# Kernel tuning notes

Measured on AMD Instinct MI355X. Metric: run time of the kernel, lower is better.

Reference implementation:

```python
import jax, jax.numpy as jnp
import numpy as np

V = 1.0e10           # large init value for non-seed pixels (FastGeodis v)
LAMB = 0.0           # lamb=0 => pure Euclidean raster-scan distance
ITERS = 2            # FastGeodis iterations
THRESH = 0.7         # binarize_map threshold
TOPO_WEIGHT = 0.005
TOPO_WINDOW = 64
EPS = 1e-6
BIG = 1e20


def _sweep_down(dist, image):
    # One top-down raster sweep of the FastGeodis up-down pass.
    # dist, image: [H, W]. Row r updates from row r-1 at col offsets {-1,0,+1}
    # with squared spatial distances {2,1,2}; lamb weights the intensity term.
    W = dist.shape[1]
    sp2 = (2.0, 1.0, 2.0)

    def step(carry, xs):
        pd, pi = carry          # previous-row distance / intensity, [W]
        d_row, i_row = xs
        pd_pad = jnp.pad(pd, 1, constant_values=BIG)
        pi_pad = jnp.pad(pi, 1, constant_values=0.0)
        new = d_row
        for k in range(3):
            p = pd_pad[k:k + W]
            q = i_row - pi_pad[k:k + W]
            new = jnp.minimum(new, p + jnp.sqrt(sp2[k] + LAMB * q * q))
        return (new, i_row), new

    (_, _), rest = jax.lax.scan(step, (dist[0], image[0]), (dist[1:], image[1:]))
    return jnp.concatenate([dist[:1], rest], axis=0)


def _updown(dist, image):
    dist = _sweep_down(dist, image)
    dist = _sweep_down(dist[::-1], image[::-1])[::-1]
    return dist


def generalised_geodesic2d(image, softmask):
    # image: intensity map [H,W]; softmask: [H,W]; dist init = V * softmask.
    dist = V * softmask
    for _ in range(ITERS):
        dist = _updown(dist, image)
        dist = _updown(dist.T, image.T).T
    return dist


def calculate_edt(inp):
    # Original: softmask = inp, intensity image = 1 - inp (mask_pt = 1 - image_pt).
    return generalised_geodesic2d(1.0 - inp, inp)


def _global_norm(x):
    return (x - x.min()) / (x.max() - x.min() + EPS)


def _topo_loss(p, t, window):
    # Persistence-style matching proxy: within each non-overlapping window,
    # match level-set values of pred and target by sorting (0-dim persistence
    # birth/death values of the filtration are order statistics of the window)
    # and penalize squared differences of matched values.
    H, W = p.shape
    nh, nw = H // window, W // window

    def win_sort(x):
        x = x.reshape(nh, window, nw, window).transpose(0, 2, 1, 3)
        return jnp.sort(x.reshape(nh * nw, window * window), axis=-1)

    return jnp.mean((win_sort(p) - win_sort(t)) ** 2)


def _per_item(pred_i, target_i):
    # pred_i/target_i: [C, H, W]; pred already remapped to [0, 1]
    bin_pred = (pred_i >= THRESH).astype(jnp.float32)
    comb_pred = jnp.max(bin_pred, axis=0)        # combine_channels
    comb_tgt = jnp.max(target_i, axis=0)
    edt_p = _global_norm(calculate_edt(1.0 - comb_pred))
    edt_t = _global_norm(calculate_edt(1.0 - comb_tgt))
    return _topo_loss(edt_p, edt_t, TOPO_WINDOW)


def setup_inputs():
    key = jax.random.key(0)
    k1, k2 = jax.random.split(key)
    B, C, H, W = 16, 3, 512, 512
    pred = jax.random.normal(k1, (B, C, H, W), dtype=jnp.float32)  # model output in ~[-1,1]
    # target: binary multi-channel cell masks (sparse foreground)
    target = (jax.random.uniform(k2, (B, C, H, W)) > 0.8).astype(jnp.float32)
    return {"pred": pred, "target": target}


def reference(pred, target):
    pred01 = (pred + 1.0) / 2.0
    losses = jax.vmap(_per_item)(pred01.astype(jnp.float32), target.astype(jnp.float32))
    mean_loss = losses.mean()
    return (mean_loss * TOPO_WEIGHT, mean_loss)
```

## Files before the change

### kernel.cpp

```cpp
#include <hip/hip_runtime.h>

#define BIGF 1e20f
#define VF   1e10f

constexpr float SQ2 = 1.41421356237309515f;

__device__ __forceinline__ float dpp_left(float x)
{
    int o = __builtin_amdgcn_update_dpp(0x60AD78ECu , __float_as_int(x),
                                        0x138, 0xF, 0xF, false);
    return __int_as_float(o);
}
__device__ __forceinline__ float dpp_right(float x)
{
    int o = __builtin_amdgcn_update_dpp(0x60AD78ECu , __float_as_int(x),
                                        0x130, 0xF, 0xF, false);
    return __int_as_float(o);
}
template<int CTRL>
__device__ __forceinline__ float qdpp(float x)
{
    return __int_as_float(__builtin_amdgcn_update_dpp(0, __float_as_int(x),
                                                      CTRL, 0xF, 0xF, true));
}
__device__ __forceinline__ float fmed3(float a, float b, float c)
{
    return __builtin_amdgcn_fmed3f(a, b, c);
}

__device__ __forceinline__ void load_row8(const float* __restrict__ M, int r, int c0, float v[8])
{
    const float4* q = (const float4*)(M + ((long)r << 9) + c0);
    float4 a = q[0], b = q[1];
    v[0] = a.x; v[1] = a.y; v[2] = a.z; v[3] = a.w;
    v[4] = b.x; v[5] = b.y; v[6] = b.z; v[7] = b.w;
}
__device__ __forceinline__ void store_row8(float* __restrict__ M, int r, int c0, const float v[8])
{
    float4* q = (float4*)(M + ((long)r << 9) + c0);
    q[0] = make_float4(v[0], v[1], v[2], v[3]);
    q[1] = make_float4(v[4], v[5], v[6], v[7]);
}

__device__ __forceinline__ void step8(const float cur[8], const float p[8], float nv[8])
{
    float left  = dpp_left(p[7]);
    float right = dpp_right(p[0]);
    #pragma unroll
    for (int j = 0; j < 8; ++j) {
        float l  = (j == 0) ? left  : p[j - 1];
        float rr = (j == 7) ? right : p[j + 1];
        nv[j] = fminf(fminf(cur[j], p[j] + 1.0f), fminf(l, rr) + SQ2);
    }
}

__global__ __launch_bounds__(256) void k_init(const float* __restrict__ pred,
                                              const float* __restrict__ tgt,
                                              float* __restrict__ bufA,
                                              float* __restrict__ acc,
                                              unsigned* __restrict__ count,
                                              float* __restrict__ minmax)
{
    if (blockIdx.x == 0 && threadIdx.x == 0) { *acc = 0.0f; *count = 0u; }
    if (blockIdx.x == 0 && threadIdx.x < 64)
        minmax[threadIdx.x] = (threadIdx.x & 1) ? 0.0f : BIGF;

    int r = blockIdx.x & 7;
    int k = blockIdx.x >> 3;
    int b = r + 8 * (k >> 10);
    int pix = (k & 1023) * 256 + threadIdx.x;
    long base = (long)b * 3 * 262144 + pix;

    float p0 = pred[base], p1 = pred[base + 262144], p2 = pred[base + 2 * 262144];
    bool fgP = ((p0 + 1.0f) * 0.5f >= 0.7f) ||
               ((p1 + 1.0f) * 0.5f >= 0.7f) ||
               ((p2 + 1.0f) * 0.5f >= 0.7f);

    float t0 = tgt[base], t1 = tgt[base + 262144], t2 = tgt[base + 2 * 262144];
    float mt = fmaxf(fmaxf(t0, t1), t2);

    bufA[(long)b * 262144 + pix]        = fgP ? 0.0f : VF;
    bufA[(long)(16 + b) * 262144 + pix] = VF * (1.0f - mt);
}

__global__ __launch_bounds__(64) void k_p1d(const float* __restrict__ X0,
                                            float* __restrict__ Cb)
{
    int bi = blockIdx.x, m = bi >> 4, w = bi & 15;
    const float* X = X0 + ((long)m << 18);
    int c0 = (int)threadIdx.x << 3, a = w << 5;
    float p[8]; load_row8(X, a, c0, p);
    float buf[8][8];
    #pragma unroll
    for (int k = 1; k <= 7; ++k) load_row8(X, a + k, c0, buf[k & 7]);
    #pragma unroll
    for (int i = 1; i < 32; ++i) {
        if (i + 7 < 32) load_row8(X, a + i + 7, c0, buf[(i + 7) & 7]);
        float nv[8]; step8(buf[i & 7], p, nv);
        #pragma unroll
        for (int j = 0; j < 8; ++j) p[j] = nv[j];
    }
    float4* o = (float4*)(Cb + m * 8192 + w * 512 + c0);
    o[0] = make_float4(p[0], p[1], p[2], p[3]);
    o[1] = make_float4(p[4], p[5], p[6], p[7]);
}

__device__ __forceinline__ void combine(float* __restrict__ bwp, float* __restrict__ part,
                                        int wdst, int wsrc, int t, int wave, int lane,
                                        const float wreg[8])
{
    const float* bs = bwp + wsrc * 576;
    if (wave <= 8) {
        int base = lane * 8 + 8 * wave;
        float W[16];
        float4 W0 = *(const float4*)(bs + base);
        float4 W1 = *(const float4*)(bs + base + 4);
        W[0]=W0.x; W[1]=W0.y; W[2]=W0.z; W[3]=W0.w;
        W[4]=W1.x; W[5]=W1.y; W[6]=W1.z; W[7]=W1.w;
        float acc[8];
        if (wave < 8) {
            float4 W2 = *(const float4*)(bs + base + 8);
            float4 W3 = *(const float4*)(bs + base + 12);
            W[8]=W2.x; W[9]=W2.y; W[10]=W2.z; W[11]=W2.w;
            W[12]=W3.x; W[13]=W3.y; W[14]=W3.z; W[15]=W3.w;
            #pragma unroll
            for (int j = 0; j < 8; ++j) acc[j] = W[j] + wreg[0];
            #pragma unroll
            for (int dt = 1; dt < 8; ++dt)
                #pragma unroll
                for (int j = 0; j < 8; ++j)
                    acc[j] = fminf(acc[j], W[j + dt] + wreg[dt]);
        } else {
            #pragma unroll
            for (int j = 0; j < 8; ++j) acc[j] = W[j] + wreg[0];
        }
        float4* pp = (float4*)(part + wave * 512 + lane * 8);
        pp[0] = make_float4(acc[0], acc[1], acc[2], acc[3]);
        pp[1] = make_float4(acc[4], acc[5], acc[6], acc[7]);
    }
    __syncthreads();
    if (t < 512) {
        float r = bwp[wdst * 576 + 32 + t];
        #pragma unroll
        for (int p2 = 0; p2 < 9; ++p2) r = fminf(r, part[p2 * 512 + t]);
        bwp[wdst * 576 + 32 + t] = r;
    }
    __syncthreads();
}

__global__ __launch_bounds__(1024) void k_comb(float* __restrict__ Cb, int dir)
{
    __shared__ __align__(16) float bwp[16 * 576];
    __shared__ __align__(16) float part[9 * 512];
    __shared__ float wgt[72];
    int m = blockIdx.x, t = threadIdx.x, wave = t >> 6, lane = t & 63, c0 = lane << 3;
    float* Cm = Cb + m * 8192;

    bwp[wave * 576 + ((lane < 32) ? lane : lane + 512)] = BIGF;
    *(float4*)(bwp + wave * 576 + 32 + c0)     = *(const float4*)(Cm + wave * 512 + c0);
    *(float4*)(bwp + wave * 576 + 32 + c0 + 4) = *(const float4*)(Cm + wave * 512 + c0 + 4);
    if (t < 65) { int d = t - 32; int ad = d < 0 ? -d : d; wgt[t] = ad * SQ2 + (float)(32 - ad); }
    __syncthreads();
    float wreg[8];
    #pragma unroll
    for (int dt = 0; dt < 8; ++dt) wreg[dt] = BIGF;
    if (wave < 8) {
        #pragma unroll
        for (int dt = 0; dt < 8; ++dt) wreg[dt] = wgt[wave * 8 + dt];
    } else if (wave == 8) wreg[0] = wgt[64];

    #pragma unroll 1
    for (int i = 0; i < 15; ++i) {
        int w2 = (dir > 0) ? (1 + i) : (14 - i);
        combine(bwp, part, w2, w2 - dir, t, wave, lane, wreg);
    }
    *(float4*)(Cm + wave * 512 + c0)     = *(const float4*)(bwp + wave * 576 + 32 + c0);
    *(float4*)(Cm + wave * 512 + c0 + 4) = *(const float4*)(bwp + wave * 576 + 32 + c0 + 4);
}

__global__ __launch_bounds__(64) void k_p3d1u(const float* __restrict__ X0,
                                              float* __restrict__ Y0,
                                              const float* __restrict__ Cb,
                                              float* __restrict__ Db)
{
    __shared__ __align__(16) float stash[31 * 512];
    int bi = blockIdx.x, m = bi >> 4, w = bi & 15;
    const float* X = X0 + ((long)m << 18);
    float* Y = Y0 + ((long)m << 18);
    const int L = threadIdx.x;
    int c0 = L << 3, a = w << 5;
    float p[8], buf[8][8];

    if (w == 0) {
        load_row8(X, 0, c0, p);
        store_row8(Y, 0, c0, p);
        *(float4*)(stash + 0 * 512 + L * 4)       = make_float4(p[0], p[1], p[2], p[3]);
        *(float4*)(stash + 0 * 512 + 256 + L * 4) = make_float4(p[4], p[5], p[6], p[7]);
        #pragma unroll
        for (int k = 1; k <= 7; ++k) load_row8(X, k, c0, buf[k & 7]);
        #pragma unroll
        for (int i = 1; i < 32; ++i) {
            if (i + 7 < 32) load_row8(X, i + 7, c0, buf[(i + 7) & 7]);
            float nv[8]; step8(buf[i & 7], p, nv);
            store_row8(Y, i, c0, nv);
            if (i < 31) {
                *(float4*)(stash + i * 512 + L * 4)       = make_float4(nv[0], nv[1], nv[2], nv[3]);
                *(float4*)(stash + i * 512 + 256 + L * 4) = make_float4(nv[4], nv[5], nv[6], nv[7]);
            }
            #pragma unroll
            for (int j = 0; j < 8; ++j) p[j] = nv[j];
        }
    } else {
        const float4* s = (const float4*)(Cb + m * 8192 + (w - 1) * 512 + c0);
        float4 s0 = s[0], s1 = s[1];
        p[0]=s0.x; p[1]=s0.y; p[2]=s0.z; p[3]=s0.w;
        p[4]=s1.x; p[5]=s1.y; p[6]=s1.z; p[7]=s1.w;
        #pragma unroll
        for (int k = 0; k < 7; ++k) load_row8(X, a + k, c0, buf[k & 7]);
        #pragma unroll
        for (int i = 0; i < 32; ++i) {
            if (i + 7 < 32) load_row8(X, a + i + 7, c0, buf[(i + 7) & 7]);
            float nv[8]; step8(buf[i & 7], p, nv);
            store_row8(Y, a + i, c0, nv);
            if (i < 31) {
                *(float4*)(stash + i * 512 + L * 4)       = make_float4(nv[0], nv[1], nv[2], nv[3]);
                *(float4*)(stash + i * 512 + 256 + L * 4) = make_float4(nv[4], nv[5], nv[6], nv[7]);
            }
            #pragma unroll
            for (int j = 0; j < 8; ++j) p[j] = nv[j];
        }
    }

    float q[8], cur[8];
    #pragma unroll
    for (int j = 0; j < 8; ++j) q[j] = p[j];
    {
        float4 x0 = *(const float4*)(stash + 30 * 512 + L * 4);
        float4 x1 = *(const float4*)(stash + 30 * 512 + 256 + L * 4);
        cur[0]=x0.x; cur[1]=x0.y; cur[2]=x0.z; cur[3]=x0.w;
        cur[4]=x1.x; cur[5]=x1.y; cur[6]=x1.z; cur[7]=x1.w;
    }
    #pragma unroll
    for (int i = 1; i < 32; ++i) {
        float nxt[8];
        if (i < 31) {
            float4 x0 = *(const float4*)(stash + (30 - i) * 512 + L * 4);
            float4 x1 = *(const float4*)(stash + (30 - i) * 512 + 256 + L * 4);
            nxt[0]=x0.x; nxt[1]=x0.y; nxt[2]=x0.z; nxt[3]=x0.w;
            nxt[4]=x1.x; nxt[5]=x1.y; nxt[6]=x1.z; nxt[7]=x1.w;
        }
        float nv[8]; step8(cur, q, nv);
        #pragma unroll
        for (int j = 0; j < 8; ++j) q[j] = nv[j];
        if (i < 31) {
            #pragma unroll
            for (int j = 0; j < 8; ++j) cur[j] = nxt[j];
        }
    }
    float4* o = (float4*)(Db + m * 8192 + w * 512 + c0);
    o[0] = make_float4(q[0], q[1], q[2], q[3]);
    o[1] = make_float4(q[4], q[5], q[6], q[7]);
}

__device__ __forceinline__ void tile_store(float* tile, int h, int c0, const float v[8])
{
    float4* q = (float4*)(tile + h * 516 + c0);
    q[0] = make_float4(v[0], v[1], v[2], v[3]);
    q[1] = make_float4(v[4], v[5], v[6], v[7]);
}
__device__ __forceinline__ void half_out(const float* tile, float* __restrict__ Xo,
                                         int a2, int L)
{
    int g = L >> 2, j = (L & 3) << 2;
    #pragma unroll
    for (int it = 0; it < 32; ++it) {
        int c = (it << 4) + g;
        float4 v = make_float4(tile[(j + 0) * 516 + c], tile[(j + 1) * 516 + c],
                               tile[(j + 2) * 516 + c], tile[(j + 3) * 516 + c]);
        *(float4*)(Xo + (long)c * 512 + a2 + j) = v;
    }
}

__global__ __launch_bounds__(64) void k_p3u(const float* __restrict__ Y0,
                                            float* __restrict__ Xo0,
                                            const float* __restrict__ Db,
                                            float* __restrict__ minmax,
                                            int final_pass)
{
    __shared__ __align__(16) float tile[16 * 516];
    int bi = blockIdx.x, m = bi >> 4, w = bi & 15;
    const float* Y = Y0 + ((long)m << 18);
    float* Xo = Xo0 + ((long)m << 18);
    int L = threadIdx.x, c0 = L << 3, a = w << 5;
    float p[8], buf[8][8];
    float mn = BIGF, mx = -BIGF;

    if (w == 15) {
        load_row8(Y, 511, c0, p);
        tile_store(tile, 15, c0, p);
        #pragma unroll
        for (int j = 0; j < 8; ++j) { mn = fminf(mn, p[j]); mx = fmaxf(mx, p[j]); }
        #pragma unroll
        for (int k = 1; k <= 7; ++k) load_row8(Y, 511 - k, c0, buf[k & 7]);
        #pragma unroll
        for (int i = 1; i < 16; ++i) {
            if (i + 7 < 32) load_row8(Y, 511 - (i + 7), c0, buf[(i + 7) & 7]);
            float nv[8]; step8(buf[i & 7], p, nv);
            tile_store(tile, 15 - i, c0, nv);
            #pragma unroll
            for (int j = 0; j < 8; ++j) { p[j] = nv[j]; mn = fminf(mn, nv[j]); mx = fmaxf(mx, nv[j]); }
        }
        half_out(tile, Xo, a + 16, L);
        #pragma unroll
        for (int i = 16; i < 32; ++i) {
            if (i + 7 < 32) load_row8(Y, 511 - (i + 7), c0, buf[(i + 7) & 7]);
            float nv[8]; step8(buf[i & 7], p, nv);
            tile_store(tile, 31 - i, c0, nv);
            #pragma unroll
            for (int j = 0; j < 8; ++j) { p[j] = nv[j]; mn = fminf(mn, nv[j]); mx = fmaxf(mx, nv[j]); }
        }
        half_out(tile, Xo, a, L);
    } else {
        const float4* s = (const float4*)(Db + m * 8192 + (w + 1) * 512 + c0);
        float4 s0 = s[0], s1 = s[1];
        p[0]=s0.x; p[1]=s0.y; p[2]=s0.z; p[3]=s0.w;
        p[4]=s1.x; p[5]=s1.y; p[6]=s1.z; p[7]=s1.w;
        #pragma unroll
        for (int k = 0; k < 7; ++k) load_row8(Y, a + 31 - k, c0, buf[k & 7]);
        #pragma unroll
        for (int i = 0; i < 16; ++i) {
            if (i + 7 < 32) load_row8(Y, a + 31 - (i + 7), c0, buf[(i + 7) & 7]);
            float nv[8]; step8(buf[i & 7], p, nv);
            tile_store(tile, 15 - i, c0, nv);
            #pragma unroll
            for (int j = 0; j < 8; ++j) { p[j] = nv[j]; mn = fminf(mn, nv[j]); mx = fmaxf(mx, nv[j]); }
        }
        half_out(tile, Xo, a + 16, L);
        #pragma unroll
        for (int i = 16; i < 32; ++i) {
            if (i + 7 < 32) load_row8(Y, a + 31 - (i + 7), c0, buf[(i + 7) & 7]);
            float nv[8]; step8(buf[i & 7], p, nv);
            tile_store(tile, 31 - i, c0, nv);
            #pragma unroll
            for (int j = 0; j < 8; ++j) { p[j] = nv[j]; mn = fminf(mn, nv[j]); mx = fmaxf(mx, nv[j]); }
        }
        half_out(tile, Xo, a, L);
    }

    if (final_pass) {
        for (int o = 32; o > 0; o >>= 1) {
            mn = fminf(mn, __shfl_down(mn, o));
            mx = fmaxf(mx, __shfl_down(mx, o));
        }
        if (L == 0) {
            atomicMin((int*)(minmax + 2 * m),     __float_as_int(mn));
            atomicMax((int*)(minmax + 2 * m + 1), __float_as_int(mx));
        }
    }
}

__device__ __forceinline__ void cex(float& lo, float& hi)
{
    float l = fminf(lo, hi);
    hi = fmaxf(lo, hi);
    lo = l;
}
__device__ __forceinline__ void merge8asc(float v[8])
{
    cex(v[0],v[4]); cex(v[1],v[5]); cex(v[2],v[6]); cex(v[3],v[7]);
    cex(v[0],v[2]); cex(v[1],v[3]); cex(v[4],v[6]); cex(v[5],v[7]);
    cex(v[0],v[1]); cex(v[2],v[3]); cex(v[4],v[5]); cex(v[6],v[7]);
}
__device__ __forceinline__ void sort8asc(float v[8])
{
    cex(v[0],v[1]); cex(v[2],v[3]); cex(v[4],v[5]); cex(v[6],v[7]);
    cex(v[0],v[3]); cex(v[1],v[2]); cex(v[4],v[7]); cex(v[5],v[6]);
    cex(v[0],v[1]); cex(v[2],v[3]); cex(v[4],v[5]); cex(v[6],v[7]);
    cex(v[0],v[7]); cex(v[1],v[6]); cex(v[2],v[5]); cex(v[3],v[4]);
    cex(v[0],v[2]); cex(v[1],v[3]); cex(v[4],v[6]); cex(v[5],v[7]);
    cex(v[0],v[1]); cex(v[2],v[3]); cex(v[4],v[5]); cex(v[6],v[7]);
}
__device__ __forceinline__ void xshfl(float v[8], int j8, float sel)
{
    #pragma unroll
    for (int e = 0; e < 8; ++e) {
        float o = __shfl_xor(v[e], j8);
        v[e] = fmed3(v[e], o, sel);
// ... 127 lines not shown
    float s = 0.0f;
    #pragma unroll
    for (int e = 0; e < 8; ++e) { float d = p[e] - q[e]; s += d * d; }
    for (int o = 32; o > 0; o >>= 1) s += __shfl_down(s, o);
    if ((t & 63) == 0) rs[t >> 6] = s;
    __syncthreads();
    if (t == 0) {
        float tot = 0.0f;
        #pragma unroll
        for (int i = 0; i < 8; ++i) tot += rs[i];
        atomicAdd(acc, tot);
        __threadfence();
        unsigned done = atomicAdd(count, 1u);
        if (done == 1023u) {
            float total = atomicAdd(acc, 0.0f);
            float mean = total * (1.0f / 4194304.0f);
            out[0] = mean * 0.005f;
            out[1] = mean;
        }
    }
}

extern "C" void kernel_launch(void* const* d_in, const int* in_sizes, int n_in,
                              void* d_out, int out_size, void* d_ws, size_t ws_size,
                              hipStream_t stream)
{
    const float* pred = (const float*)d_in[0];
    const float* tgt  = (const float*)d_in[1];
    float* out = (float*)d_out;

    char* ws = (char*)d_ws;
    float* bufA     = (float*)ws;
    float* bufB     = (float*)(ws + (32ull << 20));
    float* Cb       = (float*)(ws + (64ull << 20));
    float* Db       = (float*)(ws + (65ull << 20));
    float* minmax   = (float*)(ws + (66ull << 20));
    float* acc      = minmax + 64;
    unsigned* count = (unsigned*)(acc + 1);

    k_init<<<16 * 1024, 256, 0, stream>>>(pred, tgt, bufA, acc, count, minmax);

    for (int s = 0; s < 4; ++s) {
        k_p1d  <<<512,   64, 0, stream>>>(bufA, Cb);
        k_comb <<< 32, 1024, 0, stream>>>(Cb, +1);
        k_p3d1u<<<512,   64, 0, stream>>>(bufA, bufB, Cb, Db);
        k_comb <<< 32, 1024, 0, stream>>>(Db, -1);
        k_p3u  <<<512,   64, 0, stream>>>(bufB, bufA, Db, minmax, s == 3 ? 1 : 0);
    }

    k_loss<<<1024, 512, 0, stream>>>(bufA, minmax, acc, count, out);
}
```

Measured before the change: 406.6 us.

## Fuse per-pass sweep kernels into one persistent kernel with inter-block flag sync

Replaces the five kernels per pass (block-local sweep, two block-boundary combine kernels, down and up sweeps) with a single kernel. Blocks publish boundary rows through atomics and spin on global flags, and block 0 of each image runs the cross-block cone combine serially. Intermediate rows are kept in LDS instead of being written to and re-read from a global buffer. This removes launch overhead and global round trips, but depends on all 512 blocks being co-resident to avoid deadlock, and adds serial spin latency plus atomic traffic.

```diff
diff --git a/kernel.cpp b/kernel.cpp
--- a/kernel.cpp
+++ b/kernel.cpp
@@ -35,12 +35,6 @@
     v[0] = a.x; v[1] = a.y; v[2] = a.z; v[3] = a.w;
     v[4] = b.x; v[5] = b.y; v[6] = b.z; v[7] = b.w;
 }
-__device__ __forceinline__ void store_row8(float* __restrict__ M, int r, int c0, const float v[8])
-{
-    float4* q = (float4*)(M + ((long)r << 9) + c0);
-    q[0] = make_float4(v[0], v[1], v[2], v[3]);
-    q[1] = make_float4(v[4], v[5], v[6], v[7]);
-}
 
 __device__ __forceinline__ void step8(const float cur[8], const float p[8], float nv[8])
 {
@@ -51,6 +45,100 @@
         float l  = (j == 0) ? left  : p[j - 1];
         float rr = (j == 7) ? right : p[j + 1];
         nv[j] = fminf(fminf(cur[j], p[j] + 1.0f), fminf(l, rr) + SQ2);
+    }
+}
+
+__device__ __forceinline__ void sst_(float* st, int slot, int c0, const float v[8])
+{
+    float4* q = (float4*)(st + slot * 512 + c0);
+    q[0] = make_float4(v[0], v[1], v[2], v[3]);
+    q[1] = make_float4(v[4], v[5], v[6], v[7]);
+}
+__device__ __forceinline__ void sld_(const float* st, int slot, int c0, float v[8])
+{
+    const float4* q = (const float4*)(st + slot * 512 + c0);
+    float4 a = q[0], b = q[1];
+    v[0]=a.x; v[1]=a.y; v[2]=a.z; v[3]=a.w;
+    v[4]=b.x; v[5]=b.y; v[6]=b.z; v[7]=b.w;
+}
+
+__device__ __forceinline__ void pub_row(float* dst, int c0, const float v[8])
+{
+    #pragma unroll
+    for (int j = 0; j < 8; ++j) atomicExch(&dst[c0 + j], v[j]);
+}
+__device__ __forceinline__ void rd_row(float* src, int c0, float v[8])
+{
+    #pragma unroll
+    for (int j = 0; j < 8; ++j) v[j] = atomicAdd(&src[c0 + j], 0.0f);
+}
+
+__device__ __forceinline__ void spin_ge(unsigned* f, unsigned tgt)
+{
+    unsigned v = 0;
+    int iters = 0;
+    do {
+        if (threadIdx.x == 0) v = atomicAdd(f, 0u);
+        v = (unsigned)__shfl((int)v, 0);
+        if (v >= tgt) break;
+        __builtin_amdgcn_s_sleep(8);
+    } while (++iters < (1 << 21));
+}
+
+__device__ constexpr float coneWf(int t)
+{
+    int ad = (t < 32) ? (32 - t) : (t - 32);
+    return (float)ad * 1.41421356237309515f + (float)(32 - ad);
+}
+
+__device__ __forceinline__ void cone32_step(float prev[8], const float bw[8],
+                                            float* scratch, int L)
+{
+    int c0 = L << 3;
+    *(float4*)(scratch + c0)     = make_float4(prev[0], prev[1], prev[2], prev[3]);
+    *(float4*)(scratch + c0 + 4) = make_float4(prev[4], prev[5], prev[6], prev[7]);
+    float o[8];
+    #pragma unroll
+    for (int j = 0; j < 8; ++j) o[j] = bw[j];
+    #pragma unroll
+    for (int k = 0; k < 9; ++k) {
+        int blk = L - 4 + k;
+        bool ok = (blk >= 0) && (blk < 64);
+        int off = (ok ? blk : 0) << 3;
+        float4 x0 = *(const float4*)(scratch + off);
+        float4 x1 = *(const float4*)(scratch + off + 4);
+        float wv[8] = {x0.x, x0.y, x0.z, x0.w, x1.x, x1.y, x1.z, x1.w};
+        #pragma unroll
+        for (int e = 0; e < 8; ++e) {
+            float val = ok ? wv[e] : BIGF;
+            #pragma unroll
+            for (int j = 0; j < 8; ++j) {
+                const int t = (k - 4) * 8 + e - j + 32;
+                if (t >= 0 && t <= 64)
+                    o[j] = fminf(o[j], val + coneWf(t));
+            }
+        }
+    }
+    #pragma unroll
+    for (int j = 0; j < 8; ++j) prev[j] = o[j];
+}
+
+template<int PERM>
+__device__ __forceinline__ void half_out2(const float* st, float* __restrict__ Xo,
+                                          int a2, int L)
+{
+    int g = L >> 2, j = (L & 3) << 2;
+    #pragma unroll
+    for (int it = 0; it < 32; ++it) {
+        int c = (it << 4) + g;
+        float v[4];
+        #pragma unroll
+        for (int kk = 0; kk < 4; ++kk) {
+            int h = j + kk;
+            int slot = PERM ? ((h + 15) & 15) : (15 + h);
+            v[kk] = st[slot * 512 + c];
+        }
+        *(float4*)(Xo + (long)c * 512 + a2 + j) = make_float4(v[0], v[1], v[2], v[3]);
     }
 }
 
@@ -59,11 +147,15 @@
                                               float* __restrict__ bufA,
                                               float* __restrict__ acc,
                                               unsigned* __restrict__ count,
-                                              float* __restrict__ minmax)
+                                              float* __restrict__ minmax,
+                                              unsigned* __restrict__ flags)
 {
     if (blockIdx.x == 0 && threadIdx.x == 0) { *acc = 0.0f; *count = 0u; }
     if (blockIdx.x == 0 && threadIdx.x < 64)
         minmax[threadIdx.x] = (threadIdx.x & 1) ? 0.0f : BIGF;
+    if (blockIdx.x == 0) {
+        for (int i = threadIdx.x; i < 2048; i += 256) flags[i] = 0u;
+    }
 
     int r = blockIdx.x & 7;
     int k = blockIdx.x >> 3;
@@ -83,269 +175,157 @@
     bufA[(long)(16 + b) * 262144 + pix] = VF * (1.0f - mt);
 }
 
-__global__ __launch_bounds__(64) void k_p1d(const float* __restrict__ X0,
-                                            float* __restrict__ Cb)
-{
+__global__ __launch_bounds__(64) void k_pass(const float* __restrict__ Xin0,
+                                             float* __restrict__ Xout0,
+                                             float* __restrict__ bnd,
+                                             float* __restrict__ scn,
+                                             unsigned* __restrict__ flags,
+                                             float* __restrict__ minmax,
+                                             int pi, int final_pass)
+{
+    __shared__ __align__(16) float stash[31 * 512 + 512];
+    float* scratch = stash + 31 * 512;
+
     int bi = blockIdx.x, m = bi >> 4, w = bi & 15;
-    const float* X = X0 + ((long)m << 18);
-    int c0 = (int)threadIdx.x << 3, a = w << 5;
-    float p[8]; load_row8(X, a, c0, p);
-    float buf[8][8];
-    #pragma unroll
-    for (int k = 1; k <= 7; ++k) load_row8(X, a + k, c0, buf[k & 7]);
-    #pragma unroll
-    for (int i = 1; i < 32; ++i) {
-        if (i + 7 < 32) load_row8(X, a + i + 7, c0, buf[(i + 7) & 7]);
-        float nv[8]; step8(buf[i & 7], p, nv);
-        #pragma unroll
-        for (int j = 0; j < 8; ++j) p[j] = nv[j];
-    }
-    float4* o = (float4*)(Cb + m * 8192 + w * 512 + c0);
-    o[0] = make_float4(p[0], p[1], p[2], p[3]);
-    o[1] = make_float4(p[4], p[5], p[6], p[7]);
-}
-
-__device__ __forceinline__ void combine(float* __restrict__ bwp, float* __restrict__ part,
-                                        int wdst, int wsrc, int t, int wave, int lane,
-                                        const float wreg[8])
-{
-    const float* bs = bwp + wsrc * 576;
-    if (wave <= 8) {
-        int base = lane * 8 + 8 * wave;
-        float W[16];
-        float4 W0 = *(const float4*)(bs + base);
-        float4 W1 = *(const float4*)(bs + base + 4);
-        W[0]=W0.x; W[1]=W0.y; W[2]=W0.z; W[3]=W0.w;
-        W[4]=W1.x; W[5]=W1.y; W[6]=W1.z; W[7]=W1.w;
-        float acc[8];
-        if (wave < 8) {
-            float4 W2 = *(const float4*)(bs + base + 8);
-            float4 W3 = *(const float4*)(bs + base + 12);
-            W[8]=W2.x; W[9]=W2.y; W[10]=W2.z; W[11]=W2.w;
-            W[12]=W3.x; W[13]=W3.y; W[14]=W3.z; W[15]=W3.w;
-            #pragma unroll
-            for (int j = 0; j < 8; ++j) acc[j] = W[j] + wreg[0];
-            #pragma unroll
-            for (int dt = 1; dt < 8; ++dt)
-                #pragma unroll
-                for (int j = 0; j < 8; ++j)
-                    acc[j] = fminf(acc[j], W[j + dt] + wreg[dt]);
-        } else {
-            #pragma unroll
-            for (int j = 0; j < 8; ++j) acc[j] = W[j] + wreg[0];
-        }
-        float4* pp = (float4*)(part + wave * 512 + lane * 8);
-        pp[0] = make_float4(acc[0], acc[1], acc[2], acc[3]);
-        pp[1] = make_float4(acc[4], acc[5], acc[6], acc[7]);
-    }
-    __syncthreads();
-    if (t < 512) {
-        float r = bwp[wdst * 576 + 32 + t];
-        #pragma unroll
-        for (int p2 = 0; p2 < 9; ++p2) r = fminf(r, part[p2 * 512 + t]);
-        bwp[wdst * 576 + 32 + t] = r;
-    }
-    __syncthreads();
-}
-
-__global__ __launch_bounds__(1024) void k_comb(float* __restrict__ Cb, int dir)
-{
-    __shared__ __align__(16) float bwp[16 * 576];
-    __shared__ __align__(16) float part[9 * 512];
-    __shared__ float wgt[72];
-    int m = blockIdx.x, t = threadIdx.x, wave = t >> 6, lane = t & 63, c0 = lane << 3;
-    float* Cm = Cb + m * 8192;
-
-    bwp[wave * 576 + ((lane < 32) ? lane : lane + 512)] = BIGF;
-    *(float4*)(bwp + wave * 576 + 32 + c0)     = *(const float4*)(Cm + wave * 512 + c0);
-    *(float4*)(bwp + wave * 576 + 32 + c0 + 4) = *(const float4*)(Cm + wave * 512 + c0 + 4);
-    if (t < 65) { int d = t - 32; int ad = d < 0 ? -d : d; wgt[t] = ad * SQ2 + (float)(32 - ad); }
-    __syncthreads();
-    float wreg[8];
-    #pragma unroll
-    for (int dt = 0; dt < 8; ++dt) wreg[dt] = BIGF;
-    if (wave < 8) {
-        #pragma unroll
-        for (int dt = 0; dt < 8; ++dt) wreg[dt] = wgt[wave * 8 + dt];
-    } else if (wave == 8) wreg[0] = wgt[64];
-
-    #pragma unroll 1
-    for (int i = 0; i < 15; ++i) {
-        int w2 = (dir > 0) ? (1 + i) : (14 - i);
-        combine(bwp, part, w2, w2 - dir, t, wave, lane, wreg);
-    }
-    *(float4*)(Cm + wave * 512 + c0)     = *(const float4*)(bwp + wave * 576 + 32 + c0);
-    *(float4*)(Cm + wave * 512 + c0 + 4) = *(const float4*)(bwp + wave * 576 + 32 + c0 + 4);
-}
-
-__global__ __launch_bounds__(64) void k_p3d1u(const float* __restrict__ X0,
-                                              float* __restrict__ Y0,
-                                              const float* __restrict__ Cb,
-                                              float* __restrict__ Db)
-{
-    __shared__ __align__(16) float stash[31 * 512];
-    int bi = blockIdx.x, m = bi >> 4, w = bi & 15;
-    const float* X = X0 + ((long)m << 18);
-    float* Y = Y0 + ((long)m << 18);
+    const float* X = Xin0 + ((long)m << 18);
+    float* Xo = Xout0 + ((long)m << 18);
     const int L = threadIdx.x;
     int c0 = L << 3, a = w << 5;
-    float p[8], buf[8][8];
+    unsigned* fl = flags + (((pi << 5) | m) << 4);
+    float* bndm = bnd + (m << 13);
+    float* scnm = scn + (m << 13);
+
+    float p[8], row0[8], buf[8][8];
+
+    load_row8(X, a, c0, p);
+    #pragma unroll
+    for (int j = 0; j < 8; ++j) row0[j] = p[j];
+    #pragma unroll
+    for (int k = 1; k <= 7; ++k) {
+        load_row8(X, a + k, c0, buf[k & 7]);
+        if (w) sst_(stash, k - 1, c0, buf[k & 7]);
+    }
+    #pragma unroll
+    for (int i = 1; i < 32; ++i) {
+        if (i + 7 < 32) {
+            load_row8(X, a + i + 7, c0, buf[(i + 7) & 7]);
+            if (w) sst_(stash, i + 6, c0, buf[(i + 7) & 7]);
+        }
+        float nv[8]; step8(buf[i & 7], p, nv);
+        if (!w) sst_(stash, i - 1, c0, nv);
+        #pragma unroll
+        for (int j = 0; j < 8; ++j) p[j] = nv[j];
+    }
+    pub_row(bndm + (w << 9), c0, p);
+    __threadfence();
+    if (L == 0) atomicAdd(&fl[0], 1u);
 
     if (w == 0) {
-        load_row8(X, 0, c0, p);
-        store_row8(Y, 0, c0, p);
-        *(float4*)(stash + 0 * 512 + L * 4)       = make_float4(p[0], p[1], p[2], p[3]);
-        *(float4*)(stash + 0 * 512 + 256 + L * 4) = make_float4(p[4], p[5], p[6], p[7]);
-        #pragma unroll
-        for (int k = 1; k <= 7; ++k) load_row8(X, k, c0, buf[k & 7]);
-        #pragma unroll
+        spin_ge(&fl[0], 16u);
+        __threadfence();
+        float prev[8];
+        #pragma unroll
+        for (int j = 0; j < 8; ++j) prev[j] = p[j];
+        pub_row(scnm, c0, prev);
+        __threadfence();
+        if (L == 0) atomicExch(&fl[1], 1u);
+        #pragma unroll 1
+        for (int wp = 1; wp <= 14; ++wp) {
+            float bw[8]; rd_row(bndm + (wp << 9), c0, bw);
+            cone32_step(prev, bw, scratch, L);
+            pub_row(scnm + (wp << 9), c0, prev);
+            __threadfence();
+            if (L == 0) atomicExch(&fl[1], (unsigned)(wp + 1));
+        }
+    } else {
+        spin_ge(&fl[1], (unsigned)w);
+        __threadfence();
+        rd_row(scnm + ((w - 1) << 9), c0, p);
+        {
+            float nv[8]; step8(row0, p, nv);
+            #pragma unroll
+            for (int j = 0; j < 8; ++j) { row0[j] = nv[j]; p[j] = nv[j]; }
+        }
+        #pragma unroll 1
         for (int i = 1; i < 32; ++i) {
-            if (i + 7 < 32) load_row8(X, i + 7, c0, buf[(i + 7) & 7]);
-            float nv[8]; step8(buf[i & 7], p, nv);
-            store_row8(Y, i, c0, nv);
-            if (i < 31) {
-                *(float4*)(stash + i * 512 + L * 4)       = make_float4(nv[0], nv[1], nv[2], nv[3]);
-                *(float4*)(stash + i * 512 + 256 + L * 4) = make_float4(nv[4], nv[5], nv[6], nv[7]);
-            }
+            float cu[8]; sld_(stash, i - 1, c0, cu);
+            float nv[8]; step8(cu, p, nv);
+            sst_(stash, i - 1, c0, nv);
             #pragma unroll
             for (int j = 0; j < 8; ++j) p[j] = nv[j];
         }
+    }
+
+    float q[8];
+    #pragma unroll
+    for (int j = 0; j < 8; ++j) q[j] = p[j];
+    #pragma unroll 1
+    for (int i = 1; i < 32; ++i) {
+        float cu[8];
+        if (i < 31) sld_(stash, 30 - i, c0, cu);
+        else {
+            #pragma unroll
+            for (int j = 0; j < 8; ++j) cu[j] = row0[j];
+        }
+        float nv[8]; step8(cu, q, nv);
+        #pragma unroll
+        for (int j = 0; j < 8; ++j) q[j] = nv[j];
+    }
+    spin_ge(&fl[1], 15u);
+    pub_row(bndm + (w << 9), c0, q);
+    __threadfence();
+    if (L == 0) atomicAdd(&fl[2], 1u);
+
+    if (w == 0) {
+        spin_ge(&fl[2], 16u);
+        __threadfence();
+        float prev[8]; rd_row(bndm + (15 << 9), c0, prev);
+        pub_row(scnm + (15 << 9), c0, prev);
+        __threadfence();
+        if (L == 0) atomicExch(&fl[3], 1u);
+        #pragma unroll 1
+        for (int wp = 14; wp >= 1; --wp) {
+            float bw[8]; rd_row(bndm + (wp << 9), c0, bw);
+            cone32_step(prev, bw, scratch, L);
+            pub_row(scnm + (wp << 9), c0, prev);
+            __threadfence();
+            if (L == 0) atomicExch(&fl[3], (unsigned)(16 - wp));
+        }
+    }
+
+    float s2[8];
+    if (w == 15) {
+        #pragma unroll
+        for (int j = 0; j < 8; ++j) s2[j] = BIGF;
     } else {
-        const float4* s = (const float4*)(Cb + m * 8192 + (w - 1) * 512 + c0);
-        float4 s0 = s[0], s1 = s[1];
-        p[0]=s0.x; p[1]=s0.y; p[2]=s0.z; p[3]=s0.w;
-        p[4]=s1.x; p[5]=s1.y; p[6]=s1.z; p[7]=s1.w;
-        #pragma unroll
-        for (int k = 0; k < 7; ++k) load_row8(X, a + k, c0, buf[k & 7]);
-        #pragma unroll
-        for (int i = 0; i < 32; ++i) {
-            if (i + 7 < 32) load_row8(X, a + i + 7, c0, buf[(i + 7) & 7]);
-            float nv[8]; step8(buf[i & 7], p, nv);
-            store_row8(Y, a + i, c0, nv);
-            if (i < 31) {
-                *(float4*)(stash + i * 512 + L * 4)       = make_float4(nv[0], nv[1], nv[2], nv[3]);
-                *(float4*)(stash + i * 512 + 256 + L * 4) = make_float4(nv[4], nv[5], nv[6], nv[7]);
-            }
+        spin_ge(&fl[3], (unsigned)(15 - w));
+        __threadfence();
+        rd_row(scnm + ((w + 1) << 9), c0, s2);
+    }
+    float mn = BIGF, mx = -BIGF;
+    #pragma unroll 1
+    for (int i = 0; i < 16; ++i) {
+        float cu[8]; sld_(stash, 30 - i, c0, cu);
+        float nv[8]; step8(cu, s2, nv);
+        sst_(stash, 30 - i, c0, nv);
+        #pragma unroll
+        for (int j = 0; j < 8; ++j) { s2[j] = nv[j]; mn = fminf(mn, nv[j]); mx = fmaxf(mx, nv[j]); }
+    }
+    half_out2<0>(stash, Xo, a + 16, L);
+    #pragma unroll 1
+    for (int i = 16; i < 32; ++i) {
+        float cu[8];
+        if (i < 31) sld_(stash, 30 - i, c0, cu);
+        else {
             #pragma unroll
-            for (int j = 0; j < 8; ++j) p[j] = nv[j];
-        }
-    }
-
-    float q[8], cur[8];
-    #pragma unroll
-    for (int j = 0; j < 8; ++j) q[j] = p[j];
-    {
-        float4 x0 = *(const float4*)(stash + 30 * 512 + L * 4);
-        float4 x1 = *(const float4*)(stash + 30 * 512 + 256 + L * 4);
-        cur[0]=x0.x; cur[1]=x0.y; cur[2]=x0.z; cur[3]=x0.w;
-        cur[4]=x1.x; cur[5]=x1.y; cur[6]=x1.z; cur[7]=x1.w;
-    }
-    #pragma unroll
-    for (int i = 1; i < 32; ++i) {
-        float nxt[8];
-        if (i < 31) {
-            float4 x0 = *(const float4*)(stash + (30 - i) * 512 + L * 4);
-            float4 x1 = *(const float4*)(stash + (30 - i) * 512 + 256 + L * 4);
-            nxt[0]=x0.x; nxt[1]=x0.y; nxt[2]=x0.z; nxt[3]=x0.w;
-            nxt[4]=x1.x; nxt[5]=x1.y; nxt[6]=x1.z; nxt[7]=x1.w;
-        }
-        float nv[8]; step8(cur, q, nv);
-        #pragma unroll
-        for (int j = 0; j < 8; ++j) q[j] = nv[j];
-        if (i < 31) {
-            #pragma unroll
-            for (int j = 0; j < 8; ++j) cur[j] = nxt[j];
-        }
-    }
-    float4* o = (float4*)(Db + m * 8192 + w * 512 + c0);
-    o[0] = make_float4(q[0], q[1], q[2], q[3]);
-    o[1] = make_float4(q[4], q[5], q[6], q[7]);
-}
-
-__device__ __forceinline__ void tile_store(float* tile, int h, int c0, const float v[8])
-{
-    float4* q = (float4*)(tile + h * 516 + c0);
-    q[0] = make_float4(v[0], v[1], v[2], v[3]);
-    q[1] = make_float4(v[4], v[5], v[6], v[7]);
-}
-__device__ __forceinline__ void half_out(const float* tile, float* __restrict__ Xo,
-                                         int a2, int L)
-{
-    int g = L >> 2, j = (L & 3) << 2;
-    #pragma unroll
-    for (int it = 0; it < 32; ++it) {
-        int c = (it << 4) + g;
-        float4 v = make_float4(tile[(j + 0) * 516 + c], tile[(j + 1) * 516 + c],
-                               tile[(j + 2) * 516 + c], tile[(j + 3) * 516 + c]);
-        *(float4*)(Xo + (long)c * 512 + a2 + j) = v;
-    }
-}
-
-__global__ __launch_bounds__(64) void k_p3u(const float* __restrict__ Y0,
-                                            float* __restrict__ Xo0,
-                                            const float* __restrict__ Db,
-                                            float* __restrict__ minmax,
-                                            int final_pass)
-{
-    __shared__ __align__(16) float tile[16 * 516];
-    int bi = blockIdx.x, m = bi >> 4, w = bi & 15;
-    const float* Y = Y0 + ((long)m << 18);
-    float* Xo = Xo0 + ((long)m << 18);
-    int L = threadIdx.x, c0 = L << 3, a = w << 5;
-    float p[8], buf[8][8];
-    float mn = BIGF, mx = -BIGF;
-
-    if (w == 15) {
-        load_row8(Y, 511, c0, p);
-        tile_store(tile, 15, c0, p);
-        #pragma unroll
-        for (int j = 0; j < 8; ++j) { mn = fminf(mn, p[j]); mx = fmaxf(mx, p[j]); }
-        #pragma unroll
-        for (int k = 1; k <= 7; ++k) load_row8(Y, 511 - k, c0, buf[k & 7]);
-        #pragma unroll
-        for (int i = 1; i < 16; ++i) {
-            if (i + 7 < 32) load_row8(Y, 511 - (i + 7), c0, buf[(i + 7) & 7]);
-            float nv[8]; step8(buf[i & 7], p, nv);
-            tile_store(tile, 15 - i, c0, nv);
-            #pragma unroll
-            for (int j = 0; j < 8; ++j) { p[j] = nv[j]; mn = fminf(mn, nv[j]); mx = fmaxf(mx, nv[j]); }
-        }
-        half_out(tile, Xo, a + 16, L);
-        #pragma unroll
-        for (int i = 16; i < 32; ++i) {
-            if (i + 7 < 32) load_row8(Y, 511 - (i + 7), c0, buf[(i + 7) & 7]);
-            float nv[8]; step8(buf[i & 7], p, nv);
-            tile_store(tile, 31 - i, c0, nv);
-            #pragma unroll
-            for (int j = 0; j < 8; ++j) { p[j] = nv[j]; mn = fminf(mn, nv[j]); mx = fmaxf(mx, nv[j]); }
-        }
-        half_out(tile, Xo, a, L);
-    } else {
-        const float4* s = (const float4*)(Db + m * 8192 + (w + 1) * 512 + c0);
-        float4 s0 = s[0], s1 = s[1];
-        p[0]=s0.x; p[1]=s0.y; p[2]=s0.z; p[3]=s0.w;
-        p[4]=s1.x; p[5]=s1.y; p[6]=s1.z; p[7]=s1.w;
-        #pragma unroll
-        for (int k = 0; k < 7; ++k) load_row8(Y, a + 31 - k, c0, buf[k & 7]);
-        #pragma unroll
-        for (int i = 0; i < 16; ++i) {
-            if (i + 7 < 32) load_row8(Y, a + 31 - (i + 7), c0, buf[(i + 7) & 7]);
-            float nv[8]; step8(buf[i & 7], p, nv);
-            tile_store(tile, 15 - i, c0, nv);
-            #pragma unroll
-            for (int j = 0; j < 8; ++j) { p[j] = nv[j]; mn = fminf(mn, nv[j]); mx = fmaxf(mx, nv[j]); }
-        }
-        half_out(tile, Xo, a + 16, L);
-        #pragma unroll
-        for (int i = 16; i < 32; ++i) {
-            if (i + 7 < 32) load_row8(Y, a + 31 - (i + 7), c0, buf[(i + 7) & 7]);
-            float nv[8]; step8(buf[i & 7], p, nv);
-            tile_store(tile, 31 - i, c0, nv);
-            #pragma unroll
-            for (int j = 0; j < 8; ++j) { p[j] = nv[j]; mn = fminf(mn, nv[j]); mx = fmaxf(mx, nv[j]); }
-        }
-        half_out(tile, Xo, a, L);
-    }
+            for (int j = 0; j < 8; ++j) cu[j] = row0[j];
+        }
+        float nv[8]; step8(cu, s2, nv);
+        sst_(stash, (i < 31) ? (30 - i) : 15, c0, nv);
+        #pragma unroll
+        for (int j = 0; j < 8; ++j) { s2[j] = nv[j]; mn = fminf(mn, nv[j]); mx = fmaxf(mx, nv[j]); }
+    }
+    half_out2<1>(stash, Xo, a, L);
 
     if (final_pass) {
         for (int o = 32; o > 0; o >>= 1) {
@@ -546,20 +526,19 @@
     char* ws = (char*)d_ws;
     float* bufA     = (float*)ws;
     float* bufB     = (float*)(ws + (32ull << 20));
-    float* Cb       = (float*)(ws + (64ull << 20));
-    float* Db       = (float*)(ws + (65ull << 20));
+    float* bnd      = (float*)(ws + (64ull << 20));
+    float* scn      = (float*)(ws + (65ull << 20));
     float* minmax   = (float*)(ws + (66ull << 20));
     float* acc      = minmax + 64;
     unsigned* count = (unsigned*)(acc + 1);
-
-    k_init<<<16 * 1024, 256, 0, stream>>>(pred, tgt, bufA, acc, count, minmax);
+    unsigned* flags = (unsigned*)(ws + (66ull << 20) + 512);
+
+    k_init<<<16 * 1024, 256, 0, stream>>>(pred, tgt, bufA, acc, count, minmax, flags);
 
     for (int s = 0; s < 4; ++s) {
-        k_p1d  <<<512,   64, 0, stream>>>(bufA, Cb);
-        k_comb <<< 32, 1024, 0, stream>>>(Cb, +1);
-        k_p3d1u<<<512,   64, 0, stream>>>(bufA, bufB, Cb, Db);
-        k_comb <<< 32, 1024, 0, stream>>>(Db, -1);
-        k_p3u  <<<512,   64, 0, stream>>>(bufB, bufA, Db, minmax, s == 3 ? 1 : 0);
+        const float* in = (s & 1) ? bufB : bufA;
+        float* outb     = (s & 1) ? bufA : bufB;
+        k_pass<<<512, 64, 0, stream>>>(in, outb, bnd, scn, flags, minmax, s, (s == 3) ? 1 : 0);
     }
 
     k_loss<<<1024, 512, 0, stream>>>(bufA, minmax, acc, count, out);
```

Result: slower. 1.303 ms (+220.5%).

## Spread each row sweep across four waves with LDS halo exchange

Applied to the files above, without the earlier changes.

The three sweep kernels now use 256 threads per block, each handling 2 columns instead of one 64-lane wave handling 8 columns per lane. Neighbouring-column values at wave boundaries are exchanged through a small double-buffered shared-memory array, with a __syncthreads every row step. The aim is more parallelism and latency hiding per block with fewer serial ALU ops per lane, at the cost of a block-wide barrier on every one of the 32+ sequential row steps.

```diff
diff --git a/kernel.cpp b/kernel.cpp
--- a/kernel.cpp
+++ b/kernel.cpp
@@ -28,30 +28,29 @@
     return __builtin_amdgcn_fmed3f(a, b, c);
 }
 
-__device__ __forceinline__ void load_row8(const float* __restrict__ M, int r, int c0, float v[8])
-{
-    const float4* q = (const float4*)(M + ((long)r << 9) + c0);
-    float4 a = q[0], b = q[1];
-    v[0] = a.x; v[1] = a.y; v[2] = a.z; v[3] = a.w;
-    v[4] = b.x; v[5] = b.y; v[6] = b.z; v[7] = b.w;
-}
-__device__ __forceinline__ void store_row8(float* __restrict__ M, int r, int c0, const float v[8])
-{
-    float4* q = (float4*)(M + ((long)r << 9) + c0);
-    q[0] = make_float4(v[0], v[1], v[2], v[3]);
-    q[1] = make_float4(v[4], v[5], v[6], v[7]);
-}
-
-__device__ __forceinline__ void step8(const float cur[8], const float p[8], float nv[8])
-{
-    float left  = dpp_left(p[7]);
-    float right = dpp_right(p[0]);
-    #pragma unroll
-    for (int j = 0; j < 8; ++j) {
-        float l  = (j == 0) ? left  : p[j - 1];
-        float rr = (j == 7) ? right : p[j + 1];
-        nv[j] = fminf(fminf(cur[j], p[j] + 1.0f), fminf(l, rr) + SQ2);
-    }
+__device__ __forceinline__ void step2(const float cur[2], const float p[2],
+                                      float nv[2], float left, float right)
+{
+    nv[0] = fminf(fminf(cur[0], p[0] + 1.0f), fminf(left, p[1]) + SQ2);
+    nv[1] = fminf(fminf(cur[1], p[1] + 1.0f), fminf(p[0], right) + SQ2);
+}
+
+__device__ __forceinline__ void halo_exchange(float* hs, int pb, int wv, int ln,
+                                              const float p[2], float& l, float& r)
+{
+    if (ln == 63 && wv < 3) hs[pb * 6 + wv * 2 + 0] = p[1];
+    if (ln == 0  && wv > 0) hs[pb * 6 + (wv - 1) * 2 + 1] = p[0];
+    __syncthreads();
+    l = dpp_left(p[1]);
+    r = dpp_right(p[0]);
+    if (ln == 0  && wv > 0) l = hs[pb * 6 + (wv - 1) * 2 + 0];
+    if (ln == 63 && wv < 3) r = hs[pb * 6 + wv * 2 + 1];
+}
+
+__device__ __forceinline__ void ld2(const float* __restrict__ M, long r, int c0, float v[2])
+{
+    float2 a = *(const float2*)(M + (r << 9) + c0);
+    v[0] = a.x; v[1] = a.y;
 }
 
 __global__ __launch_bounds__(256) void k_init(const float* __restrict__ pred,
@@ -83,26 +82,28 @@
     bufA[(long)(16 + b) * 262144 + pix] = VF * (1.0f - mt);
 }
 
-__global__ __launch_bounds__(64) void k_p1d(const float* __restrict__ X0,
-                                            float* __restrict__ Cb)
-{
+__global__ __launch_bounds__(256) void k_p1d(const float* __restrict__ X0,
+                                             float* __restrict__ Cb)
+{
+    __shared__ float hs[12];
     int bi = blockIdx.x, m = bi >> 4, w = bi & 15;
     const float* X = X0 + ((long)m << 18);
-    int c0 = (int)threadIdx.x << 3, a = w << 5;
-    float p[8]; load_row8(X, a, c0, p);
-    float buf[8][8];
-    #pragma unroll
-    for (int k = 1; k <= 7; ++k) load_row8(X, a + k, c0, buf[k & 7]);
-    #pragma unroll
-    for (int i = 1; i < 32; ++i) {
-        if (i + 7 < 32) load_row8(X, a + i + 7, c0, buf[(i + 7) & 7]);
-        float nv[8]; step8(buf[i & 7], p, nv);
-        #pragma unroll
-        for (int j = 0; j < 8; ++j) p[j] = nv[j];
-    }
-    float4* o = (float4*)(Cb + m * 8192 + w * 512 + c0);
-    o[0] = make_float4(p[0], p[1], p[2], p[3]);
-    o[1] = make_float4(p[4], p[5], p[6], p[7]);
+    const int T = threadIdx.x, wv = T >> 6, ln = T & 63;
+    int c0 = T << 1, a = w << 5;
+    int pb = 0;
+    float p[2] = {BIGF, BIGF}, buf[8][2];
+    #pragma unroll
+    for (int k = 0; k < 7; ++k) ld2(X, a + k, c0, buf[k]);
+    #pragma unroll
+    for (int i = 0; i < 32; ++i) {
+        if (i + 7 < 32) ld2(X, a + i + 7, c0, buf[(i + 7) & 7]);
+        float l, r;
+        halo_exchange(hs, pb, wv, ln, p, l, r);
+        pb ^= 1;
+        float nv[2]; step2(buf[i & 7], p, nv, l, r);
+        p[0] = nv[0]; p[1] = nv[1];
+    }
+    *(float2*)(Cb + m * 8192 + w * 512 + c0) = make_float2(p[0], p[1]);
 }
 
 __device__ __forceinline__ void combine(float* __restrict__ bwp, float* __restrict__ part,
@@ -178,181 +179,131 @@
     *(float4*)(Cm + wave * 512 + c0 + 4) = *(const float4*)(bwp + wave * 576 + 32 + c0 + 4);
 }
 
-__global__ __launch_bounds__(64) void k_p3d1u(const float* __restrict__ X0,
-                                              float* __restrict__ Y0,
-                                              const float* __restrict__ Cb,
-                                              float* __restrict__ Db)
+__global__ __launch_bounds__(256) void k_p3d1u(const float* __restrict__ X0,
+                                               float* __restrict__ Y0,
+                                               const float* __restrict__ Cb,
+                                               float* __restrict__ Db)
 {
     __shared__ __align__(16) float stash[31 * 512];
+    __shared__ float hs[12];
     int bi = blockIdx.x, m = bi >> 4, w = bi & 15;
     const float* X = X0 + ((long)m << 18);
     float* Y = Y0 + ((long)m << 18);
-    const int L = threadIdx.x;
-    int c0 = L << 3, a = w << 5;
-    float p[8], buf[8][8];
-
-    if (w == 0) {
-        load_row8(X, 0, c0, p);
-        store_row8(Y, 0, c0, p);
-        *(float4*)(stash + 0 * 512 + L * 4)       = make_float4(p[0], p[1], p[2], p[3]);
-        *(float4*)(stash + 0 * 512 + 256 + L * 4) = make_float4(p[4], p[5], p[6], p[7]);
-        #pragma unroll
-        for (int k = 1; k <= 7; ++k) load_row8(X, k, c0, buf[k & 7]);
-        #pragma unroll
-        for (int i = 1; i < 32; ++i) {
-            if (i + 7 < 32) load_row8(X, i + 7, c0, buf[(i + 7) & 7]);
-            float nv[8]; step8(buf[i & 7], p, nv);
-            store_row8(Y, i, c0, nv);
-            if (i < 31) {
-                *(float4*)(stash + i * 512 + L * 4)       = make_float4(nv[0], nv[1], nv[2], nv[3]);
-                *(float4*)(stash + i * 512 + 256 + L * 4) = make_float4(nv[4], nv[5], nv[6], nv[7]);
-            }
-            #pragma unroll
-            for (int j = 0; j < 8; ++j) p[j] = nv[j];
-        }
-    } else {
-        const float4* s = (const float4*)(Cb + m * 8192 + (w - 1) * 512 + c0);
-        float4 s0 = s[0], s1 = s[1];
-        p[0]=s0.x; p[1]=s0.y; p[2]=s0.z; p[3]=s0.w;
-        p[4]=s1.x; p[5]=s1.y; p[6]=s1.z; p[7]=s1.w;
-        #pragma unroll
-        for (int k = 0; k < 7; ++k) load_row8(X, a + k, c0, buf[k & 7]);
-        #pragma unroll
-        for (int i = 0; i < 32; ++i) {
-            if (i + 7 < 32) load_row8(X, a + i + 7, c0, buf[(i + 7) & 7]);
-            float nv[8]; step8(buf[i & 7], p, nv);
-            store_row8(Y, a + i, c0, nv);
-            if (i < 31) {
-                *(float4*)(stash + i * 512 + L * 4)       = make_float4(nv[0], nv[1], nv[2], nv[3]);
-                *(float4*)(stash + i * 512 + 256 + L * 4) = make_float4(nv[4], nv[5], nv[6], nv[7]);
-            }
-            #pragma unroll
-            for (int j = 0; j < 8; ++j) p[j] = nv[j];
-        }
-    }
-
-    float q[8], cur[8];
-    #pragma unroll
-    for (int j = 0; j < 8; ++j) q[j] = p[j];
-    {
-        float4 x0 = *(const float4*)(stash + 30 * 512 + L * 4);
-        float4 x1 = *(const float4*)(stash + 30 * 512 + 256 + L * 4);
-        cur[0]=x0.x; cur[1]=x0.y; cur[2]=x0.z; cur[3]=x0.w;
-        cur[4]=x1.x; cur[5]=x1.y; cur[6]=x1.z; cur[7]=x1.w;
-    }
+    const int T = threadIdx.x, wv = T >> 6, ln = T & 63;
+    int c0 = T << 1, a = w << 5;
+    int pb = 0;
+
+    float p[2], buf[8][2];
+    if (w) {
+        float2 s = *(const float2*)(Cb + m * 8192 + (w - 1) * 512 + c0);
+        p[0] = s.x; p[1] = s.y;
+    } else { p[0] = BIGF; p[1] = BIGF; }
+
+    #pragma unroll
+    for (int k = 0; k < 7; ++k) ld2(X, a + k, c0, buf[k]);
+    #pragma unroll
+    for (int i = 0; i < 32; ++i) {
+        if (i + 7 < 32) ld2(X, a + i + 7, c0, buf[(i + 7) & 7]);
+        float l, r;
+        halo_exchange(hs, pb, wv, ln, p, l, r);
+        pb ^= 1;
+        float nv[2]; step2(buf[i & 7], p, nv, l, r);
+        *(float2*)(Y + ((long)(a + i) << 9) + c0) = make_float2(nv[0], nv[1]);
+        if (i < 31) *(float2*)(stash + i * 512 + c0) = make_float2(nv[0], nv[1]);
+        p[0] = nv[0]; p[1] = nv[1];
+    }
+
+    float q[2] = {p[0], p[1]}, cur[2];
+    { float2 v = *(const float2*)(stash + 30 * 512 + c0); cur[0] = v.x; cur[1] = v.y; }
     #pragma unroll
     for (int i = 1; i < 32; ++i) {
-        float nxt[8];
-        if (i < 31) {
-            float4 x0 = *(const float4*)(stash + (30 - i) * 512 + L * 4);
-            float4 x1 = *(const float4*)(stash + (30 - i) * 512 + 256 + L * 4);
-            nxt[0]=x0.x; nxt[1]=x0.y; nxt[2]=x0.z; nxt[3]=x0.w;
-            nxt[4]=x1.x; nxt[5]=x1.y; nxt[6]=x1.z; nxt[7]=x1.w;
-        }
-        float nv[8]; step8(cur, q, nv);
-        #pragma unroll
-        for (int j = 0; j < 8; ++j) q[j] = nv[j];
-        if (i < 31) {
-            #pragma unroll
-            for (int j = 0; j < 8; ++j) cur[j] = nxt[j];
-        }
-    }
-    float4* o = (float4*)(Db + m * 8192 + w * 512 + c0);
-    o[0] = make_float4(q[0], q[1], q[2], q[3]);
-    o[1] = make_float4(q[4], q[5], q[6], q[7]);
-}
-
-__device__ __forceinline__ void tile_store(float* tile, int h, int c0, const float v[8])
-{
-    float4* q = (float4*)(tile + h * 516 + c0);
-    q[0] = make_float4(v[0], v[1], v[2], v[3]);
-    q[1] = make_float4(v[4], v[5], v[6], v[7]);
-}
-__device__ __forceinline__ void half_out(const float* tile, float* __restrict__ Xo,
-                                         int a2, int L)
-{
-    int g = L >> 2, j = (L & 3) << 2;
-    #pragma unroll
-    for (int it = 0; it < 32; ++it) {
-        int c = (it << 4) + g;
+        float nxt[2];
+        if (i < 31) { float2 v = *(const float2*)(stash + (30 - i) * 512 + c0); nxt[0] = v.x; nxt[1] = v.y; }
+        float l, r;
+        halo_exchange(hs, pb, wv, ln, q, l, r);
+        pb ^= 1;
+        float nv[2]; step2(cur, q, nv, l, r);
+        q[0] = nv[0]; q[1] = nv[1];
+        if (i < 31) { cur[0] = nxt[0]; cur[1] = nxt[1]; }
+    }
+    *(float2*)(Db + m * 8192 + w * 512 + c0) = make_float2(q[0], q[1]);
+}
+
+__device__ __forceinline__ void half_out256(const float* tile, float* __restrict__ Xo,
+                                            int a2, int T)
+{
+    int g = (T & 63) >> 2, j = (T & 3) << 2;
+    int it0 = (T >> 6) << 3;
+    #pragma unroll
+    for (int it = 0; it < 8; ++it) {
+        int c = ((it0 + it) << 4) + g;
         float4 v = make_float4(tile[(j + 0) * 516 + c], tile[(j + 1) * 516 + c],
                                tile[(j + 2) * 516 + c], tile[(j + 3) * 516 + c]);
         *(float4*)(Xo + (long)c * 512 + a2 + j) = v;
     }
 }
 
-__global__ __launch_bounds__(64) void k_p3u(const float* __restrict__ Y0,
-                                            float* __restrict__ Xo0,
-                                            const float* __restrict__ Db,
-                                            float* __restrict__ minmax,
-                                            int final_pass)
+__global__ __launch_bounds__(256) void k_p3u(const float* __restrict__ Y0,
+                                             float* __restrict__ Xo0,
+                                             const float* __restrict__ Db,
+                                             float* __restrict__ minmax,
+                                             int final_pass)
 {
     __shared__ __align__(16) float tile[16 * 516];
+    __shared__ float hs[12];
     int bi = blockIdx.x, m = bi >> 4, w = bi & 15;
     const float* Y = Y0 + ((long)m << 18);
     float* Xo = Xo0 + ((long)m << 18);
-    int L = threadIdx.x, c0 = L << 3, a = w << 5;
-    float p[8], buf[8][8];
+    const int T = threadIdx.x, wv = T >> 6, ln = T & 63;
+    int c0 = T << 1, a = w << 5;
+    int pb = 0;
+    float p[2], buf[8][2];
     float mn = BIGF, mx = -BIGF;
 
-    if (w == 15) {
-        load_row8(Y, 511, c0, p);
-        tile_store(tile, 15, c0, p);
-        #pragma unroll
-        for (int j = 0; j < 8; ++j) { mn = fminf(mn, p[j]); mx = fmaxf(mx, p[j]); }
-        #pragma unroll
-        for (int k = 1; k <= 7; ++k) load_row8(Y, 511 - k, c0, buf[k & 7]);
-        #pragma unroll
-        for (int i = 1; i < 16; ++i) {
-            if (i + 7 < 32) load_row8(Y, 511 - (i + 7), c0, buf[(i + 7) & 7]);
-            float nv[8]; step8(buf[i & 7], p, nv);
-            tile_store(tile, 15 - i, c0, nv);
-            #pragma unroll
-            for (int j = 0; j < 8; ++j) { p[j] = nv[j]; mn = fminf(mn, nv[j]); mx = fmaxf(mx, nv[j]); }
-        }
-        half_out(tile, Xo, a + 16, L);
-        #pragma unroll
-        for (int i = 16; i < 32; ++i) {
-            if (i + 7 < 32) load_row8(Y, 511 - (i + 7), c0, buf[(i + 7) & 7]);
-            float nv[8]; step8(buf[i & 7], p, nv);
-            tile_store(tile, 31 - i, c0, nv);
-            #pragma unroll
-            for (int j = 0; j < 8; ++j) { p[j] = nv[j]; mn = fminf(mn, nv[j]); mx = fmaxf(mx, nv[j]); }
-        }
-        half_out(tile, Xo, a, L);
-    } else {
-        const float4* s = (const float4*)(Db + m * 8192 + (w + 1) * 512 + c0);
-        float4 s0 = s[0], s1 = s[1];
-        p[0]=s0.x; p[1]=s0.y; p[2]=s0.z; p[3]=s0.w;
-        p[4]=s1.x; p[5]=s1.y; p[6]=s1.z; p[7]=s1.w;
-        #pragma unroll
-        for (int k = 0; k < 7; ++k) load_row8(Y, a + 31 - k, c0, buf[k & 7]);
-        #pragma unroll
-        for (int i = 0; i < 16; ++i) {
-            if (i + 7 < 32) load_row8(Y, a + 31 - (i + 7), c0, buf[(i + 7) & 7]);
-            float nv[8]; step8(buf[i & 7], p, nv);
-            tile_store(tile, 15 - i, c0, nv);
-            #pragma unroll
-            for (int j = 0; j < 8; ++j) { p[j] = nv[j]; mn = fminf(mn, nv[j]); mx = fmaxf(mx, nv[j]); }
-        }
-        half_out(tile, Xo, a + 16, L);
-        #pragma unroll
-        for (int i = 16; i < 32; ++i) {
-            if (i + 7 < 32) load_row8(Y, a + 31 - (i + 7), c0, buf[(i + 7) & 7]);
-            float nv[8]; step8(buf[i & 7], p, nv);
-            tile_store(tile, 31 - i, c0, nv);
-            #pragma unroll
-            for (int j = 0; j < 8; ++j) { p[j] = nv[j]; mn = fminf(mn, nv[j]); mx = fmaxf(mx, nv[j]); }
-        }
-        half_out(tile, Xo, a, L);
-    }
+    if (w < 15) {
+        float2 s = *(const float2*)(Db + m * 8192 + (w + 1) * 512 + c0);
+        p[0] = s.x; p[1] = s.y;
+    } else { p[0] = BIGF; p[1] = BIGF; }
+
+    #pragma unroll
+    for (int k = 0; k < 7; ++k) ld2(Y, a + 31 - k, c0, buf[k]);
+
+    #pragma unroll
+    for (int i = 0; i < 16; ++i) {
+        if (i + 7 < 32) ld2(Y, a + 31 - (i + 7), c0, buf[(i + 7) & 7]);
+        float l, r;
+        halo_exchange(hs, pb, wv, ln, p, l, r);
+        pb ^= 1;
+        float nv[2]; step2(buf[i & 7], p, nv, l, r);
+        *(float2*)(tile + (15 - i) * 516 + c0) = make_float2(nv[0], nv[1]);
+        mn = fminf(fminf(mn, nv[0]), nv[1]);
+        mx = fmaxf(fmaxf(mx, nv[0]), nv[1]);
+        p[0] = nv[0]; p[1] = nv[1];
+    }
+    __syncthreads();
+    half_out256(tile, Xo, a + 16, T);
+    __syncthreads();
+    #pragma unroll
+    for (int i = 16; i < 32; ++i) {
+        if (i + 7 < 32) ld2(Y, a + 31 - (i + 7), c0, buf[(i + 7) & 7]);
+        float l, r;
+        halo_exchange(hs, pb, wv, ln, p, l, r);
+        pb ^= 1;
+        float nv[2]; step2(buf[i & 7], p, nv, l, r);
+        *(float2*)(tile + (31 - i) * 516 + c0) = make_float2(nv[0], nv[1]);
+        mn = fminf(fminf(mn, nv[0]), nv[1]);
+        mx = fmaxf(fmaxf(mx, nv[0]), nv[1]);
+        p[0] = nv[0]; p[1] = nv[1];
+    }
+    __syncthreads();
+    half_out256(tile, Xo, a, T);
 
     if (final_pass) {
         for (int o = 32; o > 0; o >>= 1) {
             mn = fminf(mn, __shfl_down(mn, o));
             mx = fmaxf(mx, __shfl_down(mx, o));
         }
-        if (L == 0) {
+        if (ln == 0) {
             atomicMin((int*)(minmax + 2 * m),     __float_as_int(mn));
             atomicMax((int*)(minmax + 2 * m + 1), __float_as_int(mx));
         }
@@ -555,11 +506,11 @@
     k_init<<<16 * 1024, 256, 0, stream>>>(pred, tgt, bufA, acc, count, minmax);
 
     for (int s = 0; s < 4; ++s) {
-        k_p1d  <<<512,   64, 0, stream>>>(bufA, Cb);
+        k_p1d  <<<512,  256, 0, stream>>>(bufA, Cb);
         k_comb <<< 32, 1024, 0, stream>>>(Cb, +1);
-        k_p3d1u<<<512,   64, 0, stream>>>(bufA, bufB, Cb, Db);
+        k_p3d1u<<<512,  256, 0, stream>>>(bufA, bufB, Cb, Db);
         k_comb <<< 32, 1024, 0, stream>>>(Db, -1);
-        k_p3u  <<<512,   64, 0, stream>>>(bufB, bufA, Db, minmax, s == 3 ? 1 : 0);
+        k_p3u  <<<512,  256, 0, stream>>>(bufB, bufA, Db, minmax, s == 3 ? 1 : 0);
     }
 
     k_loss<<<1024, 512, 0, stream>>>(bufA, minmax, acc, count, out);
```

Measured after the change: 427.4 us. 5.1% more time.
